# Kernel optimization log

Hardware: AMD Instinct MI355X
Metric: run time of the kernel (lower is better)

Reference implementation:

```python
import jax, jax.numpy as jnp
import numpy as np

EMB = 1024
HEADS = 16
HEAD_DIM = EMB // HEADS


def setup_inputs() -> dict:
    key = jax.random.key(0)
    ks = jax.random.split(key, 6)
    B, S = 4, 1024
    inputs = jax.random.normal(ks[0], (B, S, EMB), dtype=jnp.float32)
    # causal mask: 1.0 where attention is disallowed (added * -1e9 in the layer)
    mask = (1.0 - jnp.tril(jnp.ones((S, S), dtype=jnp.float32)))[None, None, :, :]
    scale = 1.0 / np.sqrt(EMB)
    wq = jax.random.normal(ks[1], (EMB, EMB), dtype=jnp.float32) * scale
    wk = jax.random.normal(ks[2], (EMB, EMB), dtype=jnp.float32) * scale
    wv = jax.random.normal(ks[3], (EMB, EMB), dtype=jnp.float32) * scale
    wo = jax.random.normal(ks[4], (EMB, EMB), dtype=jnp.float32) * scale
    zb = jnp.zeros((EMB,), dtype=jnp.float32)
    return {"inputs": inputs, "mask": mask, "wq": wq, "bq": zb, "wk": wk,
            "bk": zb, "wv": wv, "bv": zb, "wo": wo, "bo": zb}


def _split_heads(t, B):
    # [B, S, E] -> [B, H, S, Dh]
    return t.reshape(B, -1, HEADS, HEAD_DIM).transpose(0, 2, 1, 3)


def reference(inputs, mask, wq, bq, wk, bk, wv, bv, wo, bo):
    B = inputs.shape[0]
    q = _split_heads(inputs @ wq + bq, B)
    k = _split_heads(inputs @ wk + bk, B)
    v = _split_heads(inputs @ wv + bv, B)
    # NOTE: source divides by sqrt(sqrt(head_num)) = head_num**0.25
    scores = jnp.einsum('bhsd,bhtd->bhst', q, k) / jnp.asarray(HEADS, inputs.dtype) ** 0.25
    if mask is not None:
        scores = scores + mask * -1e9
    attn = jax.nn.softmax(scores, axis=-1)
    z = jnp.einsum('bhst,bhtd->bhsd', attn, v)
    # Faithful to source: reshape [B,H,S,Dh] -> [B,S,E] WITHOUT transposing heads back
    z = z.reshape(B, -1, EMB)
    return z @ wo + bo
```

## Files before the change

kernel.cpp:

```cpp
#include <hip/hip_runtime.h>
#include <hip/hip_bf16.h>
#include <stdint.h>

typedef __attribute__((ext_vector_type(8))) short short8;
typedef __attribute__((ext_vector_type(4))) float float4v;

#define SEQ   1024
#define NQKV  3072

__device__ __forceinline__ float bf2f(ushort h) {
    union { uint u; float f; } c; c.u = ((uint)h) << 16; return c.f;
}
__device__ __forceinline__ ushort f2bf(float f) {
    union { uint u; float f; } c; c.f = f;
    uint u = c.u;
    return (ushort)((u + 0x7fffu + ((u >> 16) & 1u)) >> 16);
}
__device__ __forceinline__ void gl2lds16(const ushort* g, ushort* l) {
    __builtin_amdgcn_global_load_lds(
        (const __attribute__((address_space(1))) unsigned int*)(g),
        (__attribute__((address_space(3))) unsigned int*)(l),
        16, 0, 0);
}

__global__ void detect_k(const uint* __restrict__ x, int* __restrict__ flag) {
    __shared__ int cnt[256];
    int h = 0;
    for (int i = threadIdx.x; i < 4096; i += 256) {
        uint w = x[i];
        uint e = (w >> 7) & 0xFFu;
        h += (e >= 100u && e <= 130u) ? 1 : 0;
    }
    cnt[threadIdx.x] = h;
    __syncthreads();
    if (threadIdx.x == 0) {
        int s = 0;
        for (int i = 0; i < 256; i++) s += cnt[i];
        flag[0] = (s > 2048) ? 0 : 1;
    }
}

__global__ __launch_bounds__(256) void xcvt_k(const void* __restrict__ x,
                                              ushort* __restrict__ xc,
                                              const int* __restrict__ flag) {
    int i = (blockIdx.x * 256 + threadIdx.x) * 4;
    if (*flag) {
        const float* xf = (const float*)x;
        float4 v = *(const float4*)(xf + i);
        ushort4 o;
        o.x = f2bf(v.x); o.y = f2bf(v.y); o.z = f2bf(v.z); o.w = f2bf(v.w);
        *(ushort4*)(xc + i) = o;
    } else {
        *(ushort4*)(xc + i) = *(const ushort4*)((const ushort*)x + i);
    }
}

__global__ void biascat_k(const void* __restrict__ bq, const void* __restrict__ bk,
                          const void* __restrict__ bv, const void* __restrict__ bo,
                          const int* __restrict__ flag, ushort* __restrict__ bout) {
    int i = blockIdx.x * 256 + threadIdx.x;
    int sel = i >> 10, j = i & 1023;
    const void* p = (sel == 0) ? bq : (sel == 1) ? bk : (sel == 2) ? bv : bo;
    bout[i] = (*flag) ? f2bf(((const float*)p)[j]) : ((const ushort*)p)[j];
}

__global__ __launch_bounds__(256) void transpose4_k(const void* __restrict__ w0,
                                                    const void* __restrict__ w1,
                                                    const void* __restrict__ w2,
                                                    const void* __restrict__ w3,
                                                    ushort* __restrict__ outall,
                                                    const int* __restrict__ flag) {
    __shared__ ushort tile[64][72];
    int z = blockIdx.z;
    const void* in = (z == 0) ? w0 : (z == 1) ? w1 : (z == 2) ? w2 : w3;
    ushort* out = outall + (size_t)z * 1024 * 1024;
    int k0 = blockIdx.x * 64;
    int n0 = blockIdx.y * 64;
    int t = threadIdx.x;
    int r = t >> 3, c = (t & 7) * 8;
    bool isf = (*flag != 0);
#pragma unroll
    for (int p = 0; p < 2; p++) {
        int rr = r + p * 32;
        if (isf) {
            const float* src = (const float*)in + (size_t)(k0 + rr) * 1024 + n0 + c;
            float4 v0 = *(const float4*)src;
            float4 v1 = *(const float4*)(src + 4);
            tile[rr][c + 0] = f2bf(v0.x); tile[rr][c + 1] = f2bf(v0.y);
            tile[rr][c + 2] = f2bf(v0.z); tile[rr][c + 3] = f2bf(v0.w);
            tile[rr][c + 4] = f2bf(v1.x); tile[rr][c + 5] = f2bf(v1.y);
            tile[rr][c + 6] = f2bf(v1.z); tile[rr][c + 7] = f2bf(v1.w);
        } else {
            uint4 v = *(const uint4*)((const ushort*)in + (size_t)(k0 + rr) * 1024 + n0 + c);
            *(uint4*)&tile[rr][c] = v;
        }
    }
    __syncthreads();
#pragma unroll
    for (int p = 0; p < 2; p++) {
        int n = r + p * 32;
        ushort vals[8];
#pragma unroll
        for (int j = 0; j < 8; j++) vals[j] = tile[c + j][n];
        *(uint4*)(out + (size_t)(n0 + n) * 1024 + k0 + c) = *(uint4*)vals;
    }
}

__global__ __launch_bounds__(256) void vtrans_k(const ushort* __restrict__ qkv,
                                                ushort* __restrict__ vt) {
    __shared__ ushort tile[64][72];
    int t0 = blockIdx.x * 64;
    int bh = blockIdx.y;
    int b = bh >> 4, h = bh & 15;
    int t = threadIdx.x;
    int r = t >> 3, c = (t & 7) * 8;
#pragma unroll
    for (int p = 0; p < 2; p++) {
        int rr = r + p * 32;
        uint4 v = *(const uint4*)(qkv + (size_t)(b * 1024 + t0 + rr) * NQKV + 2048 + h * 64 + c);
        *(uint4*)&tile[rr][c] = v;
    }
    __syncthreads();
#pragma unroll
    for (int p = 0; p < 2; p++) {
        int d = r + p * 32;
        ushort vals[8];
#pragma unroll
        for (int j = 0; j < 8; j++) vals[j] = tile[c + j][d];
        *(uint4*)(vt + ((size_t)bh * 64 + d) * 1024 + t0 + c) = *(uint4*)vals;
    }
}

template <bool DUAL>
__global__ __launch_bounds__(256) void gemm128_k(const ushort* __restrict__ A,
                                                 const ushort* __restrict__ BT,
                                                 const ushort* __restrict__ bias,
                                                 void* __restrict__ C,
                                                 const int* __restrict__ flag,
                                                 int M, int N, int K) {
    __shared__ ushort As[128 * 32];
    __shared__ ushort Bs[128 * 32];
    int n0 = blockIdx.x * 128, m0 = blockIdx.y * 128;
    int t = threadIdx.x;
    int w = t >> 6, lane = t & 63, q = lane >> 4, ln = lane & 15;
    int wr = w >> 1, wc = w & 1;

    float4v acc[4][4];
#pragma unroll
    for (int r = 0; r < 4; r++)
#pragma unroll
        for (int cc = 0; cc < 4; cc++) acc[r][cc] = (float4v){0.f, 0.f, 0.f, 0.f};

    for (int k0 = 0; k0 < K; k0 += 32) {
#pragma unroll
        for (int j = 0; j < 2; j++) {
            int c = j * 256 + t;
            int row = c >> 2, s = c & 3;
            int kc = s ^ ((row >> 1) & 3);
            gl2lds16(A + (size_t)(m0 + row) * K + k0 + kc * 8, &As[c * 8]);
            gl2lds16(BT + (size_t)(n0 + row) * K + k0 + kc * 8, &Bs[c * 8]);
        }
        __syncthreads();
        short8 af[4], bf[4];
#pragma unroll
        for (int r = 0; r < 4; r++) {
            int row = wr * 64 + r * 16 + ln;
            af[r] = *(const short8*)&As[((row << 2) | (q ^ ((row >> 1) & 3))) * 8];
            int col = wc * 64 + r * 16 + ln;
            bf[r] = *(const short8*)&Bs[((col << 2) | (q ^ ((col >> 1) & 3))) * 8];
        }
#pragma unroll
        for (int r = 0; r < 4; r++)
#pragma unroll
            for (int cc = 0; cc < 4; cc++)
                acc[r][cc] = __builtin_amdgcn_mfma_f32_16x16x32_bf16(af[r], bf[cc], acc[r][cc], 0, 0, 0);
        __syncthreads();
    }

    bool outf = DUAL && (*flag != 0);
#pragma unroll
    for (int cc = 0; cc < 4; cc++) {
        int n = n0 + wc * 64 + cc * 16 + ln;
        float bs = bf2f(bias[n]);
#pragma unroll
        for (int r = 0; r < 4; r++) {
#pragma unroll
            for (int i = 0; i < 4; i++) {
                int m = m0 + wr * 64 + r * 16 + q * 4 + i;
                float v = acc[r][cc][i] + bs;
                if (outf) ((float*)C)[(size_t)m * N + n] = v;
                else      ((ushort*)C)[(size_t)m * N + n] = f2bf(v);
            }
        }
    }
}

__global__ __launch_bounds__(256) void attn_k(const ushort* __restrict__ qkv,
                                              const ushort* __restrict__ vt,
                                              ushort* __restrict__ zp) {
    __shared__ ushort Ks[2][64 * 64];
    __shared__ ushort Vs[2][64 * 64];
    __shared__ ushort P[4][16 * 76];
    int pr = blockIdx.x;
    int bh = blockIdx.y;
    int b = bh >> 4, h = bh & 15;
    int t = threadIdx.x;
    int w = t >> 6, lane = t & 63, q = lane >> 4, ln = lane & 15;

    const float CE = 0.72134752f;

    const ushort* Qp = qkv + (size_t)(b * SEQ) * NQKV + h * 64;
    const ushort* Kp = qkv + (size_t)(b * SEQ) * NQKV + 1024 + h * 64;
    const ushort* Vt = vt + (size_t)bh * 64 * 1024;

    int c0 = t, c1 = 256 + t;
    int row0 = c0 >> 3, kc0 = (c0 & 7) ^ (row0 & 7);
    int row1 = c1 >> 3, kc1 = (c1 & 7) ^ (row1 & 7);

    for (int rep = 0; rep < 2; rep++) {
        int ti = rep ? (15 - pr) : pr;
        int sw = ti * 64 + w * 16;

        __syncthreads();

        short8 aq0 = *(const short8*)(Qp + (size_t)(sw + ln) * NQKV + q * 8);
        short8 aq1 = *(const short8*)(Qp + (size_t)(sw + ln) * NQKV + 32 + q * 8);

        float l_p[4];
        float4v o[4];
#pragma unroll
        for (int i = 0; i < 4; i++) l_p[i] = 0.f;
#pragma unroll
        for (int nb = 0; nb < 4; nb++) o[nb] = (float4v){0.f, 0.f, 0.f, 0.f};

        gl2lds16(Kp + (size_t)row0 * NQKV + kc0 * 8, &Ks[0][c0 * 8]);
        gl2lds16(Vt + (size_t)row0 * 1024 + kc0 * 8, &Vs[0][c0 * 8]);
        gl2lds16(Kp + (size_t)row1 * NQKV + kc1 * 8, &Ks[0][c1 * 8]);
        gl2lds16(Vt + (size_t)row1 * 1024 + kc1 * 8, &Vs[0][c1 * 8]);

        for (int kt = 0; kt <= ti; kt++) {
            int cur = kt & 1;
            int t0 = kt * 64;
            __syncthreads();
            if (kt < ti) {
                int nt0 = t0 + 64, nxt = cur ^ 1;
                gl2lds16(Kp + (size_t)(nt0 + row0) * NQKV + kc0 * 8, &Ks[nxt][c0 * 8]);
                gl2lds16(Vt + (size_t)row0 * 1024 + nt0 + kc0 * 8, &Vs[nxt][c0 * 8]);
                gl2lds16(Kp + (size_t)(nt0 + row1) * NQKV + kc1 * 8, &Ks[nxt][c1 * 8]);
                gl2lds16(Vt + (size_t)row1 * 1024 + nt0 + kc1 * 8, &Vs[nxt][c1 * 8]);
            }

            float4v s[4];
#pragma unroll
            for (int nb = 0; nb < 4; nb++) {
                int row = nb * 16 + ln;
                short8 kf0 = *(const short8*)&Ks[cur][((row << 3) | (q ^ (row & 7))) * 8];
                short8 kf1 = *(const short8*)&Ks[cur][((row << 3) | ((4 + q) ^ (row & 7))) * 8];
                s[nb] = (float4v){0.f, 0.f, 0.f, 0.f};
                s[nb] = __builtin_amdgcn_mfma_f32_16x16x32_bf16(aq0, kf0, s[nb], 0, 0, 0);
                s[nb] = __builtin_amdgcn_mfma_f32_16x16x32_bf16(aq1, kf1, s[nb], 0, 0, 0);
            }
            float p[4][4];
            if (kt < ti) {
#pragma unroll
                for (int nb = 0; nb < 4; nb++)
#pragma unroll
                    for (int i = 0; i < 4; i++) p[nb][i] = exp2f(s[nb][i] * CE);
            } else {
#pragma unroll
                for (int nb = 0; nb < 4; nb++)
#pragma unroll
                    for (int i = 0; i < 4; i++) {
                        int srow = sw + q * 4 + i;
                        int col = t0 + nb * 16 + ln;
                        p[nb][i] = exp2f((col <= srow) ? s[nb][i] * CE : -1e30f);
                    }
            }
#pragma unroll
            for (int i = 0; i < 4; i++)
                l_p[i] += (p[0][i] + p[1][i]) + (p[2][i] + p[3][i]);

#pragma unroll
            for (int nb = 0; nb < 4; nb++)
#pragma unroll
                for (int i = 0; i < 4; i++)
                    P[w][(q * 4 + i) * 76 + nb * 16 + ln] = f2bf(p[nb][i]);
            asm volatile("s_waitcnt lgkmcnt(0)\n" ::: "memory");
            short8 ap0 = *(const short8*)&P[w][ln * 76 + q * 8];
            short8 ap1 = *(const short8*)&P[w][ln * 76 + 32 + q * 8];
#pragma unroll
            for (int nb = 0; nb < 4; nb++) {
                int row = nb * 16 + ln;
                short8 bv0 = *(const short8*)&Vs[cur][((row << 3) | (q ^ (row & 7))) * 8];
                short8 bv1 = *(const short8*)&Vs[cur][((row << 3) | ((4 + q) ^ (row & 7))) * 8];
                o[nb] = __builtin_amdgcn_mfma_f32_16x16x32_bf16(ap0, bv0, o[nb], 0, 0, 0);
                o[nb] = __builtin_amdgcn_mfma_f32_16x16x32_bf16(ap1, bv1, o[nb], 0, 0, 0);
            }
        }

        float l_i[4];
#pragma unroll
        for (int i = 0; i < 4; i++) {
            float ssum = l_p[i];
#pragma unroll
            for (int mk = 1; mk < 16; mk <<= 1) ssum += __shfl_xor(ssum, mk, 64);
            l_i[i] = ssum;
        }
#pragma unroll
        for (int nb = 0; nb < 4; nb++) {
#pragma unroll
            for (int i = 0; i < 4; i++) {
                int srow = sw + q * 4 + i;
                int d = nb * 16 + ln;
                float z = o[nb][i] / l_i[i];
                int sp = h * 64 + (srow >> 4);
                int ep = ((srow & 15) << 6) + d;
                zp[((size_t)(b * SEQ + sp)) * 1024 + ep] = f2bf(z);
            }
        }
    }
}

extern "C" void kernel_launch(void* const* d_in, const int* in_sizes, int n_in,
                              void* d_out, int out_size, void* d_ws, size_t ws_size,
                              hipStream_t stream) {
    const void* X  = d_in[0];
    const void* wq = d_in[2];
    const void* bq = d_in[3];
    const void* wk = d_in[4];
    const void* bk = d_in[5];
    const void* wv = d_in[6];
    const void* bv = d_in[7];
    const void* wo = d_in[8];
    const void* bo = d_in[9];

    char* ws = (char*)d_ws;
    int*    flag  = (int*)ws;
    ushort* biasq = (ushort*)(ws + 4096);
    ushort* WTall = (ushort*)(ws + 12288);
    ushort* Xc    = (ushort*)(ws + 8400896);
    ushort* QKV   = (ushort*)(ws + 16789504);
    ushort* VT    = (ushort*)(ws + 41955328);
    ushort* WTo   = WTall + 3 * 1024 * 1024;
    ushort* ZP    = Xc;

    detect_k<<<1, 256, 0, stream>>>((const uint*)X, flag);
    xcvt_k<<<4096, 256, 0, stream>>>(X, Xc, flag);
    biascat_k<<<16, 256, 0, stream>>>(bq, bk, bv, bo, flag, biasq);
    transpose4_k<<<dim3(16, 16, 4), 256, 0, stream>>>(wq, wk, wv, wo, WTall, flag);
    gemm128_k<false><<<dim3(24, 32), 256, 0, stream>>>(Xc, WTall, biasq, QKV, flag, 4096, NQKV, 1024);
    vtrans_k<<<dim3(16, 64), 256, 0, stream>>>(QKV, VT);
    attn_k<<<dim3(8, 64), 256, 0, stream>>>(QKV, VT, ZP);
    gemm128_k<true><<<dim3(8, 32), 256, 0, stream>>>(ZP, WTo, biasq + 3072, d_out, flag, 4096, 1024, 1024);
}
```

Measured before the change: 208.9 us.

## Fuse V transpose into QKV GEMM epilogue and interleave paired attention row tiles

```diff
diff --git a/kernel.cpp b/kernel.cpp
--- a/kernel.cpp
+++ b/kernel.cpp
@@ -43,16 +43,13 @@
 __global__ __launch_bounds__(256) void xcvt_k(const void* __restrict__ x,
                                               ushort* __restrict__ xc,
                                               const int* __restrict__ flag) {
+    if (!*flag) return;
     int i = (blockIdx.x * 256 + threadIdx.x) * 4;
-    if (*flag) {
-        const float* xf = (const float*)x;
-        float4 v = *(const float4*)(xf + i);
-        ushort4 o;
-        o.x = f2bf(v.x); o.y = f2bf(v.y); o.z = f2bf(v.z); o.w = f2bf(v.w);
-        *(ushort4*)(xc + i) = o;
-    } else {
-        *(ushort4*)(xc + i) = *(const ushort4*)((const ushort*)x + i);
-    }
+    const float* xf = (const float*)x;
+    float4 v = *(const float4*)(xf + i);
+    ushort4 o;
+    o.x = f2bf(v.x); o.y = f2bf(v.y); o.z = f2bf(v.z); o.w = f2bf(v.w);
+    *(ushort4*)(xc + i) = o;
 }
 
 __global__ void biascat_k(const void* __restrict__ bq, const void* __restrict__ bk,
@@ -106,36 +103,13 @@
     }
 }
 
-__global__ __launch_bounds__(256) void vtrans_k(const ushort* __restrict__ qkv,
-                                                ushort* __restrict__ vt) {
-    __shared__ ushort tile[64][72];
-    int t0 = blockIdx.x * 64;
-    int bh = blockIdx.y;
-    int b = bh >> 4, h = bh & 15;
-    int t = threadIdx.x;
-    int r = t >> 3, c = (t & 7) * 8;
-#pragma unroll
-    for (int p = 0; p < 2; p++) {
-        int rr = r + p * 32;
-        uint4 v = *(const uint4*)(qkv + (size_t)(b * 1024 + t0 + rr) * NQKV + 2048 + h * 64 + c);
-        *(uint4*)&tile[rr][c] = v;
-    }
-    __syncthreads();
-#pragma unroll
-    for (int p = 0; p < 2; p++) {
-        int d = r + p * 32;
-        ushort vals[8];
-#pragma unroll
-        for (int j = 0; j < 8; j++) vals[j] = tile[c + j][d];
-        *(uint4*)(vt + ((size_t)bh * 64 + d) * 1024 + t0 + c) = *(uint4*)vals;
-    }
-}
-
-template <bool DUAL>
-__global__ __launch_bounds__(256) void gemm128_k(const ushort* __restrict__ A,
+template <bool VOUT, bool DUAL>
+__global__ __launch_bounds__(256) void gemm128_k(const ushort* __restrict__ Araw,
+                                                 const ushort* __restrict__ Aconv,
                                                  const ushort* __restrict__ BT,
                                                  const ushort* __restrict__ bias,
                                                  void* __restrict__ C,
+                                                 ushort* __restrict__ vtout,
                                                  const int* __restrict__ flag,
                                                  int M, int N, int K) {
     __shared__ ushort As[128 * 32];
@@ -144,6 +118,7 @@
     int t = threadIdx.x;
     int w = t >> 6, lane = t & 63, q = lane >> 4, ln = lane & 15;
     int wr = w >> 1, wc = w & 1;
+    const ushort* A = (*flag) ? Aconv : Araw;
 
     float4v acc[4][4];
 #pragma unroll
@@ -177,6 +152,26 @@
         __syncthreads();
     }
 
+    if (VOUT && n0 >= 2048) {
+#pragma unroll
+        for (int cc = 0; cc < 4; cc++) {
+            int n = n0 + wc * 64 + cc * 16 + ln;
+            int hd = n - 2048, hh = hd >> 6, dd = hd & 63;
+            float bs = bf2f(bias[n]);
+#pragma unroll
+            for (int r = 0; r < 4; r++) {
+                int mb = m0 + wr * 64 + r * 16 + q * 4;
+                int b = mb >> 10, srow = mb & 1023;
+                ushort4 o4;
+                o4.x = f2bf(acc[r][cc][0] + bs);
+                o4.y = f2bf(acc[r][cc][1] + bs);
+                o4.z = f2bf(acc[r][cc][2] + bs);
+                o4.w = f2bf(acc[r][cc][3] + bs);
+                *(ushort4*)(vtout + ((size_t)(b * 16 + hh) * 64 + dd) * 1024 + srow) = o4;
+            }
+        }
+        return;
+    }
     bool outf = DUAL && (*flag != 0);
 #pragma unroll
     for (int cc = 0; cc < 4; cc++) {
@@ -200,7 +195,8 @@
                                               ushort* __restrict__ zp) {
     __shared__ ushort Ks[2][64 * 64];
     __shared__ ushort Vs[2][64 * 64];
-    __shared__ ushort P[4][16 * 76];
+    __shared__ ushort PA[4][16 * 76];
+    __shared__ ushort PB[4][16 * 76];
     int pr = blockIdx.x;
     int bh = blockIdx.y;
     int b = bh >> 4, h = bh & 15;
@@ -217,106 +213,117 @@
     int row0 = c0 >> 3, kc0 = (c0 & 7) ^ (row0 & 7);
     int row1 = c1 >> 3, kc1 = (c1 & 7) ^ (row1 & 7);
 
-    for (int rep = 0; rep < 2; rep++) {
-        int ti = rep ? (15 - pr) : pr;
-        int sw = ti * 64 + w * 16;
-
+    int tiA = pr, tiB = 15 - pr;
+    int swA = tiA * 64 + w * 16, swB = tiB * 64 + w * 16;
+
+    short8 aqA0 = *(const short8*)(Qp + (size_t)(swA + ln) * NQKV + q * 8);
+    short8 aqA1 = *(const short8*)(Qp + (size_t)(swA + ln) * NQKV + 32 + q * 8);
+    short8 aqB0 = *(const short8*)(Qp + (size_t)(swB + ln) * NQKV + q * 8);
+    short8 aqB1 = *(const short8*)(Qp + (size_t)(swB + ln) * NQKV + 32 + q * 8);
+
+    float lA[4], lB[4];
+    float4v oA[4], oB[4];
+#pragma unroll
+    for (int i = 0; i < 4; i++) { lA[i] = 0.f; lB[i] = 0.f; }
+#pragma unroll
+    for (int nb = 0; nb < 4; nb++) {
+        oA[nb] = (float4v){0.f, 0.f, 0.f, 0.f};
+        oB[nb] = (float4v){0.f, 0.f, 0.f, 0.f};
+    }
+
+    gl2lds16(Kp + (size_t)row0 * NQKV + kc0 * 8, &Ks[0][c0 * 8]);
+    gl2lds16(Vt + (size_t)row0 * 1024 + kc0 * 8, &Vs[0][c0 * 8]);
+    gl2lds16(Kp + (size_t)row1 * NQKV + kc1 * 8, &Ks[0][c1 * 8]);
+    gl2lds16(Vt + (size_t)row1 * 1024 + kc1 * 8, &Vs[0][c1 * 8]);
+
+    auto tile_step = [&](int cur, int t0, int sw, short8 aq0, short8 aq1,
+                         float* lp, float4v* o, ushort* Pw, bool maskdiag) {
+        float4v s[4];
+#pragma unroll
+        for (int nb = 0; nb < 4; nb++) {
+            int row = nb * 16 + ln;
+            short8 kf0 = *(const short8*)&Ks[cur][((row << 3) | (q ^ (row & 7))) * 8];
+            short8 kf1 = *(const short8*)&Ks[cur][((row << 3) | ((4 + q) ^ (row & 7))) * 8];
+            s[nb] = (float4v){0.f, 0.f, 0.f, 0.f};
+            s[nb] = __builtin_amdgcn_mfma_f32_16x16x32_bf16(aq0, kf0, s[nb], 0, 0, 0);
+            s[nb] = __builtin_amdgcn_mfma_f32_16x16x32_bf16(aq1, kf1, s[nb], 0, 0, 0);
+        }
+        float p[4][4];
+        if (!maskdiag) {
+#pragma unroll
+            for (int nb = 0; nb < 4; nb++)
+#pragma unroll
+                for (int i = 0; i < 4; i++) p[nb][i] = exp2f(s[nb][i] * CE);
+        } else {
+#pragma unroll
+            for (int nb = 0; nb < 4; nb++)
+#pragma unroll
+                for (int i = 0; i < 4; i++) {
+                    int srow = sw + q * 4 + i;
+                    int col = t0 + nb * 16 + ln;
+                    p[nb][i] = exp2f((col <= srow) ? s[nb][i] * CE : -1e30f);
+                }
+        }
+#pragma unroll
+        for (int i = 0; i < 4; i++)
+            lp[i] += (p[0][i] + p[1][i]) + (p[2][i] + p[3][i]);
+#pragma unroll
+        for (int nb = 0; nb < 4; nb++)
+#pragma unroll
+            for (int i = 0; i < 4; i++)
+                Pw[(q * 4 + i) * 76 + nb * 16 + ln] = f2bf(p[nb][i]);
+        asm volatile("s_waitcnt lgkmcnt(0)\n" ::: "memory");
+        short8 ap0 = *(const short8*)&Pw[ln * 76 + q * 8];
+        short8 ap1 = *(const short8*)&Pw[ln * 76 + 32 + q * 8];
+#pragma unroll
+        for (int nb = 0; nb < 4; nb++) {
+            int row = nb * 16 + ln;
+            short8 bv0 = *(const short8*)&Vs[cur][((row << 3) | (q ^ (row & 7))) * 8];
+            short8 bv1 = *(const short8*)&Vs[cur][((row << 3) | ((4 + q) ^ (row & 7))) * 8];
+            o[nb] = __builtin_amdgcn_mfma_f32_16x16x32_bf16(ap0, bv0, o[nb], 0, 0, 0);
+            o[nb] = __builtin_amdgcn_mfma_f32_16x16x32_bf16(ap1, bv1, o[nb], 0, 0, 0);
+        }
+    };
+
+    for (int kt = 0; kt <= tiB; kt++) {
+        int cur = kt & 1;
+        int t0 = kt * 64;
         __syncthreads();
-
-        short8 aq0 = *(const short8*)(Qp + (size_t)(sw + ln) * NQKV + q * 8);
-        short8 aq1 = *(const short8*)(Qp + (size_t)(sw + ln) * NQKV + 32 + q * 8);
-
-        float l_p[4];
-        float4v o[4];
-#pragma unroll
-        for (int i = 0; i < 4; i++) l_p[i] = 0.f;
-#pragma unroll
-        for (int nb = 0; nb < 4; nb++) o[nb] = (float4v){0.f, 0.f, 0.f, 0.f};
-
-        gl2lds16(Kp + (size_t)row0 * NQKV + kc0 * 8, &Ks[0][c0 * 8]);
-        gl2lds16(Vt + (size_t)row0 * 1024 + kc0 * 8, &Vs[0][c0 * 8]);
-        gl2lds16(Kp + (size_t)row1 * NQKV + kc1 * 8, &Ks[0][c1 * 8]);
-        gl2lds16(Vt + (size_t)row1 * 1024 + kc1 * 8, &Vs[0][c1 * 8]);
-
-        for (int kt = 0; kt <= ti; kt++) {
-            int cur = kt & 1;
-            int t0 = kt * 64;
-            __syncthreads();
-            if (kt < ti) {
-                int nt0 = t0 + 64, nxt = cur ^ 1;
-                gl2lds16(Kp + (size_t)(nt0 + row0) * NQKV + kc0 * 8, &Ks[nxt][c0 * 8]);
-                gl2lds16(Vt + (size_t)row0 * 1024 + nt0 + kc0 * 8, &Vs[nxt][c0 * 8]);
-                gl2lds16(Kp + (size_t)(nt0 + row1) * NQKV + kc1 * 8, &Ks[nxt][c1 * 8]);
-                gl2lds16(Vt + (size_t)row1 * 1024 + nt0 + kc1 * 8, &Vs[nxt][c1 * 8]);
-            }
-
-            float4v s[4];
-#pragma unroll
-            for (int nb = 0; nb < 4; nb++) {
-                int row = nb * 16 + ln;
-                short8 kf0 = *(const short8*)&Ks[cur][((row << 3) | (q ^ (row & 7))) * 8];
-                short8 kf1 = *(const short8*)&Ks[cur][((row << 3) | ((4 + q) ^ (row & 7))) * 8];
-                s[nb] = (float4v){0.f, 0.f, 0.f, 0.f};
-                s[nb] = __builtin_amdgcn_mfma_f32_16x16x32_bf16(aq0, kf0, s[nb], 0, 0, 0);
-                s[nb] = __builtin_amdgcn_mfma_f32_16x16x32_bf16(aq1, kf1, s[nb], 0, 0, 0);
-            }
-            float p[4][4];
-            if (kt < ti) {
-#pragma unroll
-                for (int nb = 0; nb < 4; nb++)
-#pragma unroll
-                    for (int i = 0; i < 4; i++) p[nb][i] = exp2f(s[nb][i] * CE);
-            } else {
-#pragma unroll
-                for (int nb = 0; nb < 4; nb++)
-#pragma unroll
-                    for (int i = 0; i < 4; i++) {
-                        int srow = sw + q * 4 + i;
-                        int col = t0 + nb * 16 + ln;
-                        p[nb][i] = exp2f((col <= srow) ? s[nb][i] * CE : -1e30f);
-                    }
-            }
-#pragma unroll
-            for (int i = 0; i < 4; i++)
-                l_p[i] += (p[0][i] + p[1][i]) + (p[2][i] + p[3][i]);
-
-#pragma unroll
-            for (int nb = 0; nb < 4; nb++)
-#pragma unroll
-                for (int i = 0; i < 4; i++)
-                    P[w][(q * 4 + i) * 76 + nb * 16 + ln] = f2bf(p[nb][i]);
-            asm volatile("s_waitcnt lgkmcnt(0)\n" ::: "memory");
-            short8 ap0 = *(const short8*)&P[w][ln * 76 + q * 8];
-            short8 ap1 = *(const short8*)&P[w][ln * 76 + 32 + q * 8];
-#pragma unroll
-            for (int nb = 0; nb < 4; nb++) {
-                int row = nb * 16 + ln;
-                short8 bv0 = *(const short8*)&Vs[cur][((row << 3) | (q ^ (row & 7))) * 8];
-                short8 bv1 = *(const short8*)&Vs[cur][((row << 3) | ((4 + q) ^ (row & 7))) * 8];
-                o[nb] = __builtin_amdgcn_mfma_f32_16x16x32_bf16(ap0, bv0, o[nb], 0, 0, 0);
-                o[nb] = __builtin_amdgcn_mfma_f32_16x16x32_bf16(ap1, bv1, o[nb], 0, 0, 0);
-            }
-        }
-
-        float l_i[4];
+        if (kt < tiB) {
+            int nt0 = t0 + 64, nxt = cur ^ 1;
+            gl2lds16(Kp + (size_t)(nt0 + row0) * NQKV + kc0 * 8, &Ks[nxt][c0 * 8]);
+            gl2lds16(Vt + (size_t)row0 * 1024 + nt0 + kc0 * 8, &Vs[nxt][c0 * 8]);
+            gl2lds16(Kp + (size_t)(nt0 + row1) * NQKV + kc1 * 8, &Ks[nxt][c1 * 8]);
+            gl2lds16(Vt + (size_t)row1 * 1024 + nt0 + kc1 * 8, &Vs[nxt][c1 * 8]);
+        }
+        tile_step(cur, t0, swB, aqB0, aqB1, lB, oB, PB[w], kt == tiB);
+        if (kt <= tiA)
+            tile_step(cur, t0, swA, aqA0, aqA1, lA, oA, PA[w], kt == tiA);
+    }
+
+#pragma unroll
+    for (int i = 0; i < 4; i++) {
+        float sA = lA[i], sB = lB[i];
+#pragma unroll
+        for (int mk = 1; mk < 16; mk <<= 1) {
+            sA += __shfl_xor(sA, mk, 64);
+            sB += __shfl_xor(sB, mk, 64);
+        }
+        lA[i] = sA; lB[i] = sB;
+    }
+#pragma unroll
+    for (int nb = 0; nb < 4; nb++) {
 #pragma unroll
         for (int i = 0; i < 4; i++) {
-            float ssum = l_p[i];
-#pragma unroll
-            for (int mk = 1; mk < 16; mk <<= 1) ssum += __shfl_xor(ssum, mk, 64);
-            l_i[i] = ssum;
-        }
-#pragma unroll
-        for (int nb = 0; nb < 4; nb++) {
-#pragma unroll
-            for (int i = 0; i < 4; i++) {
-                int srow = sw + q * 4 + i;
-                int d = nb * 16 + ln;
-                float z = o[nb][i] / l_i[i];
-                int sp = h * 64 + (srow >> 4);
-                int ep = ((srow & 15) << 6) + d;
-                zp[((size_t)(b * SEQ + sp)) * 1024 + ep] = f2bf(z);
-            }
+            int d = nb * 16 + ln;
+            int srowA = swA + q * 4 + i;
+            int spA = h * 64 + (srowA >> 4);
+            int epA = ((srowA & 15) << 6) + d;
+            zp[((size_t)(b * SEQ + spA)) * 1024 + epA] = f2bf(oA[nb][i] / lA[i]);
+            int srowB = swB + q * 4 + i;
+            int spB = h * 64 + (srowB >> 4);
+            int epB = ((srowB & 15) << 6) + d;
+            zp[((size_t)(b * SEQ + spB)) * 1024 + epB] = f2bf(oB[nb][i] / lB[i]);
         }
     }
 }
@@ -348,8 +355,9 @@
     xcvt_k<<<4096, 256, 0, stream>>>(X, Xc, flag);
     biascat_k<<<16, 256, 0, stream>>>(bq, bk, bv, bo, flag, biasq);
     transpose4_k<<<dim3(16, 16, 4), 256, 0, stream>>>(wq, wk, wv, wo, WTall, flag);
-    gemm128_k<false><<<dim3(24, 32), 256, 0, stream>>>(Xc, WTall, biasq, QKV, flag, 4096, NQKV, 1024);
-    vtrans_k<<<dim3(16, 64), 256, 0, stream>>>(QKV, VT);
+    gemm128_k<true, false><<<dim3(24, 32), 256, 0, stream>>>(
+        (const ushort*)X, Xc, WTall, biasq, QKV, VT, flag, 4096, NQKV, 1024);
     attn_k<<<dim3(8, 64), 256, 0, stream>>>(QKV, VT, ZP);
-    gemm128_k<true><<<dim3(8, 32), 256, 0, stream>>>(ZP, WTo, biasq + 3072, d_out, flag, 4096, 1024, 1024);
-}
+    gemm128_k<false, true><<<dim3(8, 32), 256, 0, stream>>>(
+        ZP, ZP, WTo, biasq + 3072, d_out, nullptr, flag, 4096, 1024, 1024);
+}
```

Measured after the change: 219.8 us. 5.2% more time.
